# Performance work log

Hardware: AMD Instinct MI355X
Metric: run time of the kernel (lower is better)

Reference implementation:

```python
import jax, jax.numpy as jnp
import numpy as np

K_CHEB = 3  # Chebyshev order K -> K+1 basis matrices, gcn order = K


def setup_inputs() -> dict:
    key = jax.random.key(0)
    ks = jax.random.split(key, 7)
    B, N, T, Cin, Cout, ndim = 32, 512, 12, 64, 64, 40
    support_len = K_CHEB + 1
    cin_total = (K_CHEB * support_len + 1) * Cin  # (order*support_len+1)*c_in = 832
    x = jax.random.normal(ks[0], (B, N, T, Cin), jnp.float32)
    adj = (jax.random.uniform(ks[1], (N, N)) < 0.05).astype(jnp.float32)
    adjacency = jnp.maximum(adj, jnp.eye(N, dtype=jnp.float32))
    embedding = jax.random.uniform(ks[2], (N, ndim), dtype=jnp.float32)  # nn.init.uniform_
    W1 = jax.random.normal(ks[3], (ndim, ndim // 2), jnp.float32) * 0.3
    W2 = jax.random.normal(ks[4], (ndim, ndim // 2), jnp.float32) * 0.3
    mlp_w = jax.random.normal(ks[5], (Cout, cin_total), jnp.float32) / np.float32(np.sqrt(cin_total))
    mlp_b = jnp.zeros((Cout,), jnp.float32)
    return {"x": x, "adjacency": adjacency, "embedding": embedding,
            "W1": W1, "W2": W2, "mlp_w": mlp_w, "mlp_b": mlp_b}


def _cheb_kernels(adjacency, embedding, W1, W2):
    # adaptive adjacency: embedding mixed through column-softmaxed projections
    e1 = embedding @ jax.nn.softmax(W1, axis=0)
    e2 = embedding @ jax.nn.softmax(W2, axis=0)
    e1 = e1 / (jnp.linalg.norm(e1, axis=1, keepdims=True) + 1e-8)
    e2 = e2 / (jnp.linalg.norm(e2, axis=1, keepdims=True) + 1e-8)
    weight = e1 @ e2.T  # (N, N)
    A = jnp.where(adjacency > 0.0, weight + adjacency, jnp.asarray(9e-15, adjacency.dtype))
    # symmetric normalization: L = I - D^-1/2 A D^-1/2 ; Ls = (2/maxeig)*L - I with maxeig=2 -> Ls = -sym(A)
    d = 1.0 / jnp.sqrt(A.sum(axis=1))
    Ls = -(d[:, None] * A * d[None, :])
    I = jnp.eye(A.shape[0], dtype=A.dtype)
    kernels = [I, Ls]
    for _ in range(1, K_CHEB):  # Chebyshev recursion: T_{k+1} = 2 Ls T_k - T_{k-1}
        kernels.append(2.0 * (Ls @ kernels[-1]) - kernels[-2])
    return kernels  # K_CHEB + 1 matrices of (N, N)


def reference(x, adjacency, embedding, W1, W2, mlp_w, mlp_b):
    supports = _cheb_kernels(adjacency, embedding, W1, W2)
    xp = jnp.transpose(x, (0, 3, 1, 2))  # (B, Cin, N, T)
    out = [xp]
    for a in supports:
        x1 = jnp.einsum('bcvt,vw->bcwt', xp, a)
        out.append(x1)
        for _ in range(2, K_CHEB + 1):  # gcn order = K_CHEB
            x1 = jnp.einsum('bcvt,vw->bcwt', x1, a)
            out.append(x1)
    h = jnp.concatenate(out, axis=1)  # (B, 832, N, T)
    h = jnp.einsum('bcvt,oc->bovt', h, mlp_w) + mlp_b[None, :, None, None]  # 1x1 conv
    h = jnp.transpose(h, (0, 2, 3, 1))  # (B, N, T, Cout)
    return jax.nn.relu(h + x)  # conv_r is None (Cin == Cout), dropout eval no-op
```

## Files before the change

kernel.cpp:

```cpp
#include <hip/hip_runtime.h>
#include <hip/hip_bf16.h>

typedef unsigned short ushortT;
typedef unsigned int uintT;
typedef __attribute__((ext_vector_type(8))) short bf16x8;
typedef __attribute__((ext_vector_type(4))) float f32x4;
typedef __attribute__((ext_vector_type(4))) unsigned short us4;
typedef __attribute__((ext_vector_type(8))) unsigned short us8;

__device__ __forceinline__ ushortT f2bf(float f) {
    union { float f; uintT u; } x; x.f = f;
    uintT r = x.u + 0x7fffu + ((x.u >> 16) & 1u);
    return (ushortT)(r >> 16);
}
__device__ __forceinline__ float bf2f(ushortT u) {
    union { uintT u; float f; } x; x.u = ((uintT)u) << 16; return x.f;
}

#define ZLD 260
#define KTOT 5120

__global__ __launch_bounds__(256) void k_embed(const float* __restrict__ emb,
                                               const float* __restrict__ W1,
                                               const float* __restrict__ W2,
                                               float* __restrict__ e1,
                                               float* __restrict__ e2) {
    __shared__ float sW[800];
    __shared__ float sWs[800];
    const float* W = (blockIdx.x == 0) ? W1 : W2;
    float* e = (blockIdx.x == 0) ? e1 : e2;
    int tid = threadIdx.x;
    for (int i = tid; i < 800; i += 256) sW[i] = W[i];
    __syncthreads();
    if (tid < 20) {
        float mx = -1e30f;
        for (int i = 0; i < 40; ++i) mx = fmaxf(mx, sW[i * 20 + tid]);
        float s = 0.f;
        for (int i = 0; i < 40; ++i) s += __expf(sW[i * 20 + tid] - mx);
        float inv = 1.f / s;
        for (int i = 0; i < 40; ++i) sWs[i * 20 + tid] = __expf(sW[i * 20 + tid] - mx) * inv;
    }
    __syncthreads();
    for (int row = tid; row < 512; row += 256) {
        float acc[20];
        #pragma unroll
        for (int j = 0; j < 20; ++j) acc[j] = 0.f;
        for (int i = 0; i < 40; ++i) {
            float ev = emb[row * 40 + i];
            #pragma unroll
            for (int j = 0; j < 20; ++j) acc[j] += ev * sWs[i * 20 + j];
        }
        float s = 0.f;
        #pragma unroll
        for (int j = 0; j < 20; ++j) s += acc[j] * acc[j];
        float scale = 1.f / (sqrtf(s) + 1e-8f);
        #pragma unroll
        for (int j = 0; j < 20; ++j) e[row * 20 + j] = acc[j] * scale;
    }
}

__global__ __launch_bounds__(256) void k_adj(const float* __restrict__ adj,
                                             const float* __restrict__ e1,
                                             const float* __restrict__ e2,
                                             float* __restrict__ A,
                                             float* __restrict__ d) {
    int v = blockIdx.x, tid = threadIdx.x;
    __shared__ float ev[20];
    if (tid < 20) ev[tid] = e1[v * 20 + tid];
    __syncthreads();
    float local = 0.f;
    for (int w = tid; w < 512; w += 256) {
        float dot = 0.f;
        #pragma unroll
        for (int j = 0; j < 20; ++j) dot += ev[j] * e2[w * 20 + j];
        float av = adj[v * 512 + w];
        float Av = (av > 0.f) ? (dot + av) : 9e-15f;
        A[v * 512 + w] = Av;
        local += Av;
    }
    __shared__ float red[256];
    red[tid] = local;
    __syncthreads();
    for (int s = 128; s > 0; s >>= 1) {
        if (tid < s) red[tid] += red[tid + s];
        __syncthreads();
    }
    if (tid == 0) d[v] = 1.f / sqrtf(red[0]);
}

__global__ __launch_bounds__(256) void k_m(const float* __restrict__ A,
                                           const float* __restrict__ d,
                                           ushortT* __restrict__ P,
                                           const float* __restrict__ mlp_w,
                                           ushortT* __restrict__ Wq) {
    int bx = blockIdx.x, tid = threadIdx.x;
    if (bx < 512) {
        int w = bx;
        float dw = d[w];
        for (int v = tid; v < 512; v += 256) {
            float val = -d[v] * dw * A[v * 512 + w];
            P[512 * 512 + w * 512 + v] = f2bf(val);
            P[w * 512 + v] = (v == w) ? (ushortT)0x3F80 : (ushortT)0;
        }
    } else {
        int idx = (bx - 512) * 256 + tid;
        if (idx >= 10 * 64 * 64) return;
        int q = idx >> 12, rem = idx & 4095, o = rem >> 6, c = rem & 63;
        float v;
        if (q == 0) {
            v = 0.f;
            #pragma unroll
            for (int k = 0; k < 4; ++k) v += mlp_w[o * 832 + k * 64 + c];
        } else {
            v = mlp_w[o * 832 + (q + 3) * 64 + c];
        }
        Wq[idx] = f2bf(v);
    }
}

__global__ __launch_bounds__(256) void k_gemm512(const ushortT* __restrict__ A,
                                                 const ushortT* __restrict__ B,
                                                 ushortT* __restrict__ out1,
                                                 ushortT* __restrict__ out2,
                                                 int mode,
                                                 const ushortT* __restrict__ aux,
                                                 const ushortT* __restrict__ A2,
                                                 const ushortT* __restrict__ B2,
                                                 ushortT* __restrict__ out3) {
    int bx = blockIdx.x;
    if (bx >= 64) { A = A2; B = B2; out1 = out3; out2 = nullptr; mode = 0; bx -= 64; }
    int wave = threadIdx.x >> 6, lane = threadIdx.x & 63;
    int lr = lane & 15, lg = lane >> 4;
    int mbase = (bx >> 3) * 64;
    int nbase = (bx & 7) * 64 + wave * 16;
    f32x4 acc[4] = {};
    for (int kk = 0; kk < 16; ++kk) {
        int k0 = kk * 32 + lg * 8;
        bf16x8 bfr;
        #pragma unroll
        for (int j = 0; j < 8; ++j) bfr[j] = (short)B[(k0 + j) * 512 + nbase + lr];
        #pragma unroll
        for (int wt = 0; wt < 4; ++wt) {
            bf16x8 af = *(const bf16x8*)(A + (mbase + wt * 16 + lr) * 512 + k0);
            acc[wt] = __builtin_amdgcn_mfma_f32_16x16x32_bf16(af, bfr, acc[wt], 0, 0, 0);
        }
    }
    #pragma unroll
    for (int wt = 0; wt < 4; ++wt)
        #pragma unroll
        for (int r = 0; r < 4; ++r) {
            int row = mbase + wt * 16 + lg * 4 + r;
            int col = nbase + lr;
            float v = acc[wt][r];
            out1[row * 512 + col] = f2bf(v);
            if (mode == 1) out2[row * 512 + col] = f2bf(2.f * v - (row == col ? 1.f : 0.f));
            else if (mode == 2) out2[row * 512 + col] = f2bf(4.f * v - 3.f * bf2f(aux[row * 512 + col]));
        }
}

__global__ __launch_bounds__(256) void k_z(const float* __restrict__ x,
                                           const ushortT* __restrict__ Wq,
                                           ushortT* __restrict__ Z,
                                           int slab0) {
    __shared__ ushortT Zl[64 * ZLD];
    int bid = blockIdx.x;
    int btl = bid >> 1, chunk = bid & 1;
    int bt = slab0 + btl;
    int b = bt / 12, t = bt - b * 12;
    int tid = threadIdx.x, wave = tid >> 6, lane = tid & 63;
    int lr = lane & 15, lg = lane >> 4;

    bf16x8 xn[4][2];
    const float* xb = x + ((size_t)b * 512 * 12 + t) * 64;
    #pragma unroll
    for (int vt = 0; vt < 4; ++vt) {
        int vrow = chunk * 256 + wave * 64 + vt * 16 + lr;
        const float* px = xb + (size_t)vrow * 768 + lg * 8;
        f32x4 f0 = *(const f32x4*)px;
        f32x4 f1 = *(const f32x4*)(px + 4);
        f32x4 f2 = *(const f32x4*)(px + 32);
        f32x4 f3 = *(const f32x4*)(px + 36);
        bf16x8 v0, v1;
        v0[0] = (short)f2bf(f0[0]); v0[1] = (short)f2bf(f0[1]);
        v0[2] = (short)f2bf(f0[2]); v0[3] = (short)f2bf(f0[3]);
        v0[4] = (short)f2bf(f1[0]); v0[5] = (short)f2bf(f1[1]);
        v0[6] = (short)f2bf(f1[2]); v0[7] = (short)f2bf(f1[3]);
        v1[0] = (short)f2bf(f2[0]); v1[1] = (short)f2bf(f2[1]);
        v1[2] = (short)f2bf(f2[2]); v1[3] = (short)f2bf(f2[3]);
        v1[4] = (short)f2bf(f3[0]); v1[5] = (short)f2bf(f3[1]);
        v1[6] = (short)f2bf(f3[2]); v1[7] = (short)f2bf(f3[3]);
        xn[vt][0] = v0;
        xn[vt][1] = v1;
    }

    #pragma unroll 1
    for (int q = 0; q < 10; ++q) {
        const ushortT* wqp = Wq + q * 4096;
        #pragma unroll
        for (int ot = 0; ot < 4; ++ot) {
            int o = ot * 16 + lr;
            bf16x8 wf0 = *(const bf16x8*)(wqp + o * 64 + lg * 8);
            bf16x8 wf1 = *(const bf16x8*)(wqp + o * 64 + 32 + lg * 8);
            #pragma unroll
            for (int vt = 0; vt < 4; ++vt) {
                f32x4 z = {};
                z = __builtin_amdgcn_mfma_f32_16x16x32_bf16(xn[vt][0], wf0, z, 0, 0, 0);
                z = __builtin_amdgcn_mfma_f32_16x16x32_bf16(xn[vt][1], wf1, z, 0, 0, 0);
                us4 pk = { f2bf(z[0]), f2bf(z[1]), f2bf(z[2]), f2bf(z[3]) };
                *(us4*)&Zl[o * ZLD + wave * 64 + vt * 16 + lg * 4] = pk;
            }
        }
        __syncthreads();
        size_t kbase = (size_t)q * 512 + chunk * 256;
        #pragma unroll
        for (int j = 0; j < 8; ++j) {
            int flat = j * 256 + tid;
            int o = flat >> 5, slot = flat & 31;
            us4 lo = *(const us4*)&Zl[o * ZLD + slot * 8];
            us4 hi = *(const us4*)&Zl[o * ZLD + slot * 8 + 4];
            us8 val = { lo[0], lo[1], lo[2], lo[3], hi[0], hi[1], hi[2], hi[3] };
            *(us8*)&Z[(size_t)(btl * 64 + o) * KTOT + kbase + slot * 8] = val;
        }
        __syncthreads();
    }
}

__global__ __launch_bounds__(256) void k_big(const ushortT* __restrict__ P,
                                             const ushortT* __restrict__ Z,
                                             const float* __restrict__ x,
                                             const float* __restrict__ bias,
                                             float* __restrict__ out,
                                             int slab0) {
    __shared__ ushortT SA[3][4096];
    __shared__ ushortT SB[3][4096];
    int nwg = (int)gridDim.x;
    int bid = (int)blockIdx.x;
    int cpx = nwg >> 3;
    int lbid = (bid & 7) * cpx + (bid >> 3);
    int mblk = lbid & 3;
    int nblk = lbid >> 2;
    int mbase = mblk * 128;
    int n0 = nblk * 128;
    int tid = threadIdx.x, wave = tid >> 6, lane = tid & 63;
    int lr = lane & 15, lg = lane >> 4;
    int wm = wave >> 1, wn = wave & 1;
    int srow = tid >> 2, sg = tid & 3;

    f32x4 acc[4][4] = {};

    auto stage = [&](int kt, int buf) {
        int q = kt >> 4;
        int v0 = (kt & 15) * 32;
        const ushortT* Pk = P + (size_t)q * 262144 + v0 + sg * 8;
        const ushortT* Zk = Z + (size_t)kt * 32 + sg * 8;
        #pragma unroll
        for (int i = 0; i < 2; ++i) {
            int row = i * 64 + srow;
            __builtin_amdgcn_global_load_lds(Pk + (size_t)(mbase + row) * 512,
                                             &SA[buf][(i * 256 + wave * 64) * 8], 16, 0, 0);
            __builtin_amdgcn_global_load_lds(Zk + (size_t)(n0 + row) * KTOT,
                                             &SB[buf][(i * 256 + wave * 64) * 8], 16, 0, 0);
        }
    };

    auto phase = [&](int kt) {
        int buf = kt % 3;
        bf16x8 af[4], bfr[4];
        #pragma unroll
        for (int mt = 0; mt < 4; ++mt) {
            int m = wm * 64 + mt * 16 + lr;
            af[mt] = *(const bf16x8*)&SA[buf][m * 32 + lg * 8];
        }
        #pragma unroll
        for (int nt = 0; nt < 4; ++nt) {
            int n = wn * 64 + nt * 16 + lr;
            bfr[nt] = *(const bf16x8*)&SB[buf][n * 32 + lg * 8];
        }
        bool more = (kt + 2 < 160);
        if (more) stage(kt + 2, (kt + 2) % 3);
        asm volatile("s_waitcnt lgkmcnt(0)" ::: "memory");
        __builtin_amdgcn_sched_barrier(0);
        __builtin_amdgcn_s_setprio(1);
        #pragma unroll
        for (int mt = 0; mt < 4; ++mt)
            #pragma unroll
            for (int nt = 0; nt < 4; ++nt)
                acc[mt][nt] = __builtin_amdgcn_mfma_f32_16x16x32_bf16(af[mt], bfr[nt], acc[mt][nt], 0, 0, 0);
        __builtin_amdgcn_s_setprio(0);
        __builtin_amdgcn_sched_barrier(0);
        if (more) asm volatile("s_waitcnt vmcnt(4)" ::: "memory");
        else      asm volatile("s_waitcnt vmcnt(0)" ::: "memory");
        __builtin_amdgcn_sched_barrier(0);
        __builtin_amdgcn_s_barrier();
        __builtin_amdgcn_sched_barrier(0);
    };

    stage(0, 0);
    stage(1, 1);
    asm volatile("s_waitcnt vmcnt(0)" ::: "memory");
    __builtin_amdgcn_sched_barrier(0);
    __builtin_amdgcn_s_barrier();
    __builtin_amdgcn_sched_barrier(0);

    #pragma unroll 1
    for (int kt = 0; kt < 160; ++kt) phase(kt);

    #pragma unroll
    for (int mt = 0; mt < 4; ++mt)
        #pragma unroll
        for (int nt = 0; nt < 4; ++nt)
            #pragma unroll
            for (int r = 0; r < 4; ++r) {
                int m = mbase + wm * 64 + mt * 16 + lg * 4 + r;
                int nf = n0 + wn * 64 + nt * 16 + lr;
                int btl = nf >> 6, o = nf & 63;
                int bt = slab0 + btl;
                int bb = bt / 12, t = bt - bb * 12;
                size_t oi = (((size_t)bb * 512 + m) * 12 + t) * 64 + o;
                float v = acc[mt][nt][r] + x[oi] + bias[o];
                out[oi] = (v > 0.f) ? v : 0.f;
            }
}

__global__ __launch_bounds__(256, 2) void k_main_fb(const float* __restrict__ x,
                                                    const ushortT* __restrict__ P,
                                                    const ushortT* __restrict__ Wq,
                                                    const float* __restrict__ bias,
                                                    float* __restrict__ out) {
    __shared__ ushortT Zt[64 * ZLD];
    const int SZ = 512 * 512;
    int bid = blockIdx.x;
    int slot = bid & 7, idx = bid >> 3;
    int half = slot >> 2;
    int bt = idx * 4 + (slot & 3);
    int b = bt / 12, tt = bt - b * 12;
    int tid = threadIdx.x, wave = tid >> 6, lane = tid & 63;
    int lr = lane & 15, lg = lane >> 4;
    int wbase = half * 256 + wave * 64;
    int vzb = wave * 64;
    const float* xqf = x + ((size_t)b * 512 * 12 + tt) * 64;

    f32x4 oacc[4][4] = {};
    bf16x8 xn[4][2];

    auto xload = [&](int ch) {
        #pragma unroll
        for (int vt = 0; vt < 4; ++vt) {
            int vrow = ch * 256 + vzb + vt * 16 + lr;
            const float* px = xqf + (size_t)vrow * 768 + lg * 8;
            f32x4 f0 = *(const f32x4*)px;
            f32x4 f1 = *(const f32x4*)(px + 4);
            f32x4 f2 = *(const f32x4*)(px + 32);
            f32x4 f3 = *(const f32x4*)(px + 36);
            bf16x8 v0, v1;
            v0[0] = (short)f2bf(f0[0]); v0[1] = (short)f2bf(f0[1]);
            v0[2] = (short)f2bf(f0[2]); v0[3] = (short)f2bf(f0[3]);
            v0[4] = (short)f2bf(f1[0]); v0[5] = (short)f2bf(f1[1]);
            v0[6] = (short)f2bf(f1[2]); v0[7] = (short)f2bf(f1[3]);
            v1[0] = (short)f2bf(f2[0]); v1[1] = (short)f2bf(f2[1]);
            v1[2] = (short)f2bf(f2[2]); v1[3] = (short)f2bf(f2[3]);
            v1[4] = (short)f2bf(f3[0]); v1[5] = (short)f2bf(f3[1]);
            v1[6] = (short)f2bf(f3[2]); v1[7] = (short)f2bf(f3[3]);
            xn[vt][0] = v0;
            xn[vt][1] = v1;
        }
    };
    auto zphase = [&](int q) {
        const ushortT* wqp = Wq + q * 4096;
        #pragma unroll
        for (int vt = 0; vt < 4; ++vt)
            #pragma unroll
            for (int ot = 0; ot < 4; ++ot) {
                int o = ot * 16 + lr;
                bf16x8 wf0 = *(const bf16x8*)(wqp + o * 64 + lg * 8);
                bf16x8 wf1 = *(const bf16x8*)(wqp + o * 64 + 32 + lg * 8);
                f32x4 z = {};
                z = __builtin_amdgcn_mfma_f32_16x16x32_bf16(xn[vt][0], wf0, z, 0, 0, 0);
                z = __builtin_amdgcn_mfma_f32_16x16x32_bf16(xn[vt][1], wf1, z, 0, 0, 0);
                us4 pk = { f2bf(z[0]), f2bf(z[1]), f2bf(z[2]), f2bf(z[3]) };
                *(us4*)&Zt[o * ZLD + vzb + vt * 16 + lg * 4] = pk;
            }
    };
    auto pptr = [&](int j, int mt) -> const ushortT* {
        int q = 1 + (j >> 1), ch = j & 1;
        return P + (size_t)q * SZ + (size_t)(wbase + mt * 16 + lr) * 512 + ch * 256 + lg * 8;
    };

    xload(half);
    zphase(0);
    xload(0);
    __syncthreads();
    #pragma unroll
    for (int mt = 0; mt < 4; ++mt)
        #pragma unroll
        for (int ot = 0; ot < 4; ++ot) {
            int o = ot * 16 + lr;
            us4 z4 = *(const us4*)&Zt[o * ZLD + wave * 64 + mt * 16 + lg * 4];
            oacc[mt][ot][0] = bf2f(z4[0]);
            oacc[mt][ot][1] = bf2f(z4[1]);
            oacc[mt][ot][2] = bf2f(z4[2]);
            oacc[mt][ot][3] = bf2f(z4[3]);
        }
    __syncthreads();

    #pragma unroll 1
    for (int j = 0; j < 18; ++j) {
        int q = 1 + (j >> 1);
        zphase(q);
        int jn = (j < 17) ? j + 1 : 17;
        xload(jn & 1);
        __syncthreads();
        const ushortT* pc0 = pptr(j, 0);
        const ushortT* pc1 = pptr(j, 1);
        const ushortT* pc2 = pptr(j, 2);
        const ushortT* pc3 = pptr(j, 3);
        #pragma unroll
        for (int kk = 0; kk < 8; ++kk) {
            bf16x8 a0 = *(const bf16x8*)(pc0 + kk * 32);
            bf16x8 a1 = *(const bf16x8*)(pc1 + kk * 32);
            bf16x8 a2 = *(const bf16x8*)(pc2 + kk * 32);
            bf16x8 a3 = *(const bf16x8*)(pc3 + kk * 32);
            int vb = kk * 32 + lg * 8;
            bf16x8 b0 = *(const bf16x8*)&Zt[(0 * 16 + lr) * ZLD + vb];
            bf16x8 b1 = *(const bf16x8*)&Zt[(1 * 16 + lr) * ZLD + vb];
            bf16x8 b2 = *(const bf16x8*)&Zt[(2 * 16 + lr) * ZLD + vb];
            bf16x8 b3 = *(const bf16x8*)&Zt[(3 * 16 + lr) * ZLD + vb];
            oacc[0][0] = __builtin_amdgcn_mfma_f32_16x16x32_bf16(a0, b0, oacc[0][0], 0, 0, 0);
            oacc[1][0] = __builtin_amdgcn_mfma_f32_16x16x32_bf16(a1, b0, oacc[1][0], 0, 0, 0);
            oacc[2][0] = __builtin_amdgcn_mfma_f32_16x16x32_bf16(a2, b0, oacc[2][0], 0, 0, 0);
            oacc[3][0] = __builtin_amdgcn_mfma_f32_16x16x32_bf16(a3, b0, oacc[3][0], 0, 0, 0);
            oacc[0][1] = __builtin_amdgcn_mfma_f32_16x16x32_bf16(a0, b1, oacc[0][1], 0, 0, 0);
            oacc[1][1] = __builtin_amdgcn_mfma_f32_16x16x32_bf16(a1, b1, oacc[1][1], 0, 0, 0);
            oacc[2][1] = __builtin_amdgcn_mfma_f32_16x16x32_bf16(a2, b1, oacc[2][1], 0, 0, 0);
            oacc[3][1] = __builtin_amdgcn_mfma_f32_16x16x32_bf16(a3, b1, oacc[3][1], 0, 0, 0);
            oacc[0][2] = __builtin_amdgcn_mfma_f32_16x16x32_bf16(a0, b2, oacc[0][2], 0, 0, 0);
            oacc[1][2] = __builtin_amdgcn_mfma_f32_16x16x32_bf16(a1, b2, oacc[1][2], 0, 0, 0);
            oacc[2][2] = __builtin_amdgcn_mfma_f32_16x16x32_bf16(a2, b2, oacc[2][2], 0, 0, 0);
            oacc[3][2] = __builtin_amdgcn_mfma_f32_16x16x32_bf16(a3, b2, oacc[3][2], 0, 0, 0);
            oacc[0][3] = __builtin_amdgcn_mfma_f32_16x16x32_bf16(a0, b3, oacc[0][3], 0, 0, 0);
            oacc[1][3] = __builtin_amdgcn_mfma_f32_16x16x32_bf16(a1, b3, oacc[1][3], 0, 0, 0);
            oacc[2][3] = __builtin_amdgcn_mfma_f32_16x16x32_bf16(a2, b3, oacc[2][3], 0, 0, 0);
            oacc[3][3] = __builtin_amdgcn_mfma_f32_16x16x32_bf16(a3, b3, oacc[3][3], 0, 0, 0);
        }
        __syncthreads();
    }

    #pragma unroll
    for (int mt = 0; mt < 4; ++mt)
        #pragma unroll
        for (int ot = 0; ot < 4; ++ot)
            #pragma unroll
            for (int r = 0; r < 4; ++r) {
                int w = wbase + mt * 16 + lg * 4 + r;
                int o = ot * 16 + lr;
                size_t oi = (((size_t)b * 512 + w) * 12 + tt) * 64 + o;
                float v = oacc[mt][ot][r] + x[oi] + bias[o];
                out[oi] = (v > 0.f) ? v : 0.f;
            }
}

extern "C" void kernel_launch(void* const* d_in, const int* in_sizes, int n_in,
                              void* d_out, int out_size, void* d_ws, size_t ws_size,
                              hipStream_t stream) {
    const float* x    = (const float*)d_in[0];
    const float* adj  = (const float*)d_in[1];
    const float* emb  = (const float*)d_in[2];
    const float* W1   = (const float*)d_in[3];
    const float* W2   = (const float*)d_in[4];
    const float* mlpw = (const float*)d_in[5];
    const float* mlpb = (const float*)d_in[6];
    float* out = (float*)d_out;

    char* ws = (char*)d_ws;
    float*   e1   = (float*)(ws + 0);
    float*   e2   = (float*)(ws + 65536);
    float*   A    = (float*)(ws + 131072);
    float*   dvec = (float*)(ws + 1179648);
    ushortT* P    = (ushortT*)(ws + 1183744);
    ushortT* Wq   = (ushortT*)(ws + 6426624);
    ushortT* Z    = (ushortT*)(ws + 6508544);
    const size_t ZOFF = 6508544;

    k_embed<<<2, 256, 0, stream>>>(emb, W1, W2, e1, e2);
    k_adj<<<512, 256, 0, stream>>>(adj, e1, e2, A, dvec);
    k_m<<<672, 256, 0, stream>>>(A, dvec, P, mlpw, Wq);

    const int SZ = 512 * 512;
    ushortT *S1 = P + 1 * SZ, *S2 = P + 2 * SZ, *S3 = P + 3 * SZ, *S4 = P + 4 * SZ,
            *S5 = P + 5 * SZ, *S6 = P + 6 * SZ, *S7 = P + 7 * SZ, *S8 = P + 8 * SZ,
            *S9 = P + 9 * SZ;
    k_gemm512<<<64, 256, 0, stream>>>(S1, S1, S2, S4, 1, nullptr, nullptr, nullptr, nullptr);
    k_gemm512<<<128, 256, 0, stream>>>(S1, S2, S3, S7, 2, S1, S4, S4, S5);
    k_gemm512<<<128, 256, 0, stream>>>(S4, S5, S6, nullptr, 0, nullptr, S7, S7, S8);
    k_gemm512<<<64, 256, 0, stream>>>(S7, S8, S9, nullptr, 0, nullptr, nullptr, nullptr, nullptr);

    const size_t ZFULL = (size_t)24576 * KTOT * 2;
    int nslab = 1;
    while (nslab <= 8 && ws_size < ZOFF + ZFULL / (size_t)nslab) nslab <<= 1;

    if (nslab <= 8) {
        int btps = 384 / nslab;
        for (int s = 0; s < nslab; ++s) {
            k_z<<<btps * 2, 256, 0, stream>>>(x, Wq, Z, s * btps);
            k_big<<<btps * 2, 256, 0, stream>>>(P, Z, x, mlpb, out, s * btps);
        }
    } else {
        k_main_fb<<<768, 256, 0, stream>>>(x, P, Wq, mlpb, out);
    }
    (void)in_sizes; (void)n_in; (void)out_size;
}
```

Baseline: 373.0 us.

## Deepen k_big pipeline to four LDS buffers and pre-convert x to bf16

The main GEMM kernel moves from a 3-stage to a 4-stage LDS ring, prefetching three k-tiles ahead and placing the vmcnt wait and barrier at the start of each phase, so global loads get more time to land before use. A new prep kernel converts x to bf16 in a (bt, v, c) layout when the workspace is large enough, so k_z reads contiguous bf16 rows instead of strided fp32 with inline conversion. The costs are more LDS per block (64KB), which may lower occupancy, an extra kernel launch, and a full extra pass over x.

```diff
diff --git a/kernel.cpp b/kernel.cpp
--- a/kernel.cpp
+++ b/kernel.cpp
@@ -118,6 +118,101 @@
     }
 }
 
+__global__ __launch_bounds__(256) void k_prep(const float* __restrict__ x,
+                                              ushortT* __restrict__ xbf) {
+    size_t i = (size_t)blockIdx.x * 256 + threadIdx.x;
+    int c = (int)(i & 15) * 4;
+    int v = (int)((i >> 4) & 511);
+    int bt = (int)(i >> 13);
+    int b = bt / 12, t = bt - b * 12;
+    f32x4 f = *(const f32x4*)(x + (((size_t)b * 512 + v) * 12 + t) * 64 + c);
+    us4 o = { f2bf(f[0]), f2bf(f[1]), f2bf(f[2]), f2bf(f[3]) };
+    *(us4*)(xbf + ((size_t)bt * 512 + v) * 64 + c) = o;
+}
+
+template<bool XBF>
+__device__ void kz_body(const float* __restrict__ x,
+                        const ushortT* __restrict__ xbf,
+                        const ushortT* __restrict__ Wq,
+                        ushortT* __restrict__ Z,
+                        int kzbid, int slab0) {
+    __shared__ ushortT Zl[64 * ZLD];
+    int btl = kzbid >> 1, chunk = kzbid & 1;
+    int bt = slab0 + btl;
+    int b = bt / 12, t = bt - b * 12;
+    int tid = threadIdx.x, wave = tid >> 6, lane = tid & 63;
+    int lr = lane & 15, lg = lane >> 4;
+
+    bf16x8 xn[4][2];
+    const float* xb = x + ((size_t)b * 512 * 12 + t) * 64;
+    const ushortT* xq = xbf + (size_t)bt * 512 * 64;
+    #pragma unroll
+    for (int vt = 0; vt < 4; ++vt) {
+        int vrow = chunk * 256 + wave * 64 + vt * 16 + lr;
+        if (XBF) {
+            xn[vt][0] = *(const bf16x8*)(xq + vrow * 64 + lg * 8);
+            xn[vt][1] = *(const bf16x8*)(xq + vrow * 64 + 32 + lg * 8);
+        } else {
+            const float* px = xb + (size_t)vrow * 768 + lg * 8;
+            f32x4 f0 = *(const f32x4*)px;
+            f32x4 f1 = *(const f32x4*)(px + 4);
+            f32x4 f2 = *(const f32x4*)(px + 32);
+            f32x4 f3 = *(const f32x4*)(px + 36);
+            bf16x8 v0, v1;
+            v0[0] = (short)f2bf(f0[0]); v0[1] = (short)f2bf(f0[1]);
+            v0[2] = (short)f2bf(f0[2]); v0[3] = (short)f2bf(f0[3]);
+            v0[4] = (short)f2bf(f1[0]); v0[5] = (short)f2bf(f1[1]);
+            v0[6] = (short)f2bf(f1[2]); v0[7] = (short)f2bf(f1[3]);
+            v1[0] = (short)f2bf(f2[0]); v1[1] = (short)f2bf(f2[1]);
+            v1[2] = (short)f2bf(f2[2]); v1[3] = (short)f2bf(f2[3]);
+            v1[4] = (short)f2bf(f3[0]); v1[5] = (short)f2bf(f3[1]);
+            v1[6] = (short)f2bf(f3[2]); v1[7] = (short)f2bf(f3[3]);
+            xn[vt][0] = v0;
+            xn[vt][1] = v1;
+        }
+    }
+
+    #pragma unroll 1
+    for (int q = 0; q < 10; ++q) {
+        const ushortT* wqp = Wq + q * 4096;
+        #pragma unroll
+        for (int ot = 0; ot < 4; ++ot) {
+            int o = ot * 16 + lr;
+            bf16x8 wf0 = *(const bf16x8*)(wqp + o * 64 + lg * 8);
+            bf16x8 wf1 = *(const bf16x8*)(wqp + o * 64 + 32 + lg * 8);
+            #pragma unroll
+            for (int vt = 0; vt < 4; ++vt) {
+                f32x4 z = {};
+                z = __builtin_amdgcn_mfma_f32_16x16x32_bf16(xn[vt][0], wf0, z, 0, 0, 0);
+                z = __builtin_amdgcn_mfma_f32_16x16x32_bf16(xn[vt][1], wf1, z, 0, 0, 0);
+                us4 pk = { f2bf(z[0]), f2bf(z[1]), f2bf(z[2]), f2bf(z[3]) };
+                *(us4*)&Zl[o * ZLD + wave * 64 + vt * 16 + lg * 4] = pk;
+            }
+        }
+        __syncthreads();
+        size_t kbase = (size_t)q * 512 + chunk * 256;
+        #pragma unroll
+        for (int j = 0; j < 8; ++j) {
+            int flat = j * 256 + tid;
+            int o = flat >> 5, slot = flat & 31;
+            us4 lo = *(const us4*)&Zl[o * ZLD + slot * 8];
+            us4 hi = *(const us4*)&Zl[o * ZLD + slot * 8 + 4];
+            us8 val = { lo[0], lo[1], lo[2], lo[3], hi[0], hi[1], hi[2], hi[3] };
+            *(us8*)&Z[(size_t)(btl * 64 + o) * KTOT + kbase + slot * 8] = val;
+        }
+        __syncthreads();
+    }
+}
+
+template<bool XBF>
+__global__ __launch_bounds__(256) void k_z(const float* __restrict__ x,
+                                           const ushortT* __restrict__ xbf,
+                                           const ushortT* __restrict__ Wq,
+                                           ushortT* __restrict__ Z,
+                                           int slab0) {
+    kz_body<XBF>(x, xbf, Wq, Z, blockIdx.x, slab0);
+}
+
 __global__ __launch_bounds__(256) void k_gemm512(const ushortT* __restrict__ A,
                                                  const ushortT* __restrict__ B,
                                                  ushortT* __restrict__ out1,
@@ -158,81 +253,14 @@
         }
 }
 
-__global__ __launch_bounds__(256) void k_z(const float* __restrict__ x,
-                                           const ushortT* __restrict__ Wq,
-                                           ushortT* __restrict__ Z,
-                                           int slab0) {
-    __shared__ ushortT Zl[64 * ZLD];
-    int bid = blockIdx.x;
-    int btl = bid >> 1, chunk = bid & 1;
-    int bt = slab0 + btl;
-    int b = bt / 12, t = bt - b * 12;
-    int tid = threadIdx.x, wave = tid >> 6, lane = tid & 63;
-    int lr = lane & 15, lg = lane >> 4;
-
-    bf16x8 xn[4][2];
-    const float* xb = x + ((size_t)b * 512 * 12 + t) * 64;
-    #pragma unroll
-    for (int vt = 0; vt < 4; ++vt) {
-        int vrow = chunk * 256 + wave * 64 + vt * 16 + lr;
-        const float* px = xb + (size_t)vrow * 768 + lg * 8;
-        f32x4 f0 = *(const f32x4*)px;
-        f32x4 f1 = *(const f32x4*)(px + 4);
-        f32x4 f2 = *(const f32x4*)(px + 32);
-        f32x4 f3 = *(const f32x4*)(px + 36);
-        bf16x8 v0, v1;
-        v0[0] = (short)f2bf(f0[0]); v0[1] = (short)f2bf(f0[1]);
-        v0[2] = (short)f2bf(f0[2]); v0[3] = (short)f2bf(f0[3]);
-        v0[4] = (short)f2bf(f1[0]); v0[5] = (short)f2bf(f1[1]);
-        v0[6] = (short)f2bf(f1[2]); v0[7] = (short)f2bf(f1[3]);
-        v1[0] = (short)f2bf(f2[0]); v1[1] = (short)f2bf(f2[1]);
-        v1[2] = (short)f2bf(f2[2]); v1[3] = (short)f2bf(f2[3]);
-        v1[4] = (short)f2bf(f3[0]); v1[5] = (short)f2bf(f3[1]);
-        v1[6] = (short)f2bf(f3[2]); v1[7] = (short)f2bf(f3[3]);
-        xn[vt][0] = v0;
-        xn[vt][1] = v1;
-    }
-
-    #pragma unroll 1
-    for (int q = 0; q < 10; ++q) {
-        const ushortT* wqp = Wq + q * 4096;
-        #pragma unroll
-        for (int ot = 0; ot < 4; ++ot) {
-            int o = ot * 16 + lr;
-            bf16x8 wf0 = *(const bf16x8*)(wqp + o * 64 + lg * 8);
-            bf16x8 wf1 = *(const bf16x8*)(wqp + o * 64 + 32 + lg * 8);
-            #pragma unroll
-            for (int vt = 0; vt < 4; ++vt) {
-                f32x4 z = {};
-                z = __builtin_amdgcn_mfma_f32_16x16x32_bf16(xn[vt][0], wf0, z, 0, 0, 0);
-                z = __builtin_amdgcn_mfma_f32_16x16x32_bf16(xn[vt][1], wf1, z, 0, 0, 0);
-                us4 pk = { f2bf(z[0]), f2bf(z[1]), f2bf(z[2]), f2bf(z[3]) };
-                *(us4*)&Zl[o * ZLD + wave * 64 + vt * 16 + lg * 4] = pk;
-            }
-        }
-        __syncthreads();
-        size_t kbase = (size_t)q * 512 + chunk * 256;
-        #pragma unroll
-        for (int j = 0; j < 8; ++j) {
-            int flat = j * 256 + tid;
-            int o = flat >> 5, slot = flat & 31;
-            us4 lo = *(const us4*)&Zl[o * ZLD + slot * 8];
-            us4 hi = *(const us4*)&Zl[o * ZLD + slot * 8 + 4];
-            us8 val = { lo[0], lo[1], lo[2], lo[3], hi[0], hi[1], hi[2], hi[3] };
-            *(us8*)&Z[(size_t)(btl * 64 + o) * KTOT + kbase + slot * 8] = val;
-        }
-        __syncthreads();
-    }
-}
-
 __global__ __launch_bounds__(256) void k_big(const ushortT* __restrict__ P,
                                              const ushortT* __restrict__ Z,
                                              const float* __restrict__ x,
                                              const float* __restrict__ bias,
                                              float* __restrict__ out,
                                              int slab0) {
-    __shared__ ushortT SA[3][4096];
-    __shared__ ushortT SB[3][4096];
+    __shared__ ushortT SA[4][4096];
+    __shared__ ushortT SB[4][4096];
     int nwg = (int)gridDim.x;
     int bid = (int)blockIdx.x;
     int cpx = nwg >> 3;
@@ -263,8 +291,14 @@
         }
     };
 
-    auto phase = [&](int kt) {
-        int buf = kt % 3;
+    auto phase = [&](int kt, int wsel) {
+        if (wsel == 0)      asm volatile("s_waitcnt vmcnt(8)" ::: "memory");
+        else if (wsel == 1) asm volatile("s_waitcnt vmcnt(4)" ::: "memory");
+        else                asm volatile("s_waitcnt vmcnt(0)" ::: "memory");
+        __builtin_amdgcn_sched_barrier(0);
+        __builtin_amdgcn_s_barrier();
+        __builtin_amdgcn_sched_barrier(0);
+        int buf = kt & 3;
         bf16x8 af[4], bfr[4];
         #pragma unroll
         for (int mt = 0; mt < 4; ++mt) {
@@ -276,10 +310,7 @@
             int n = wn * 64 + nt * 16 + lr;
             bfr[nt] = *(const bf16x8*)&SB[buf][n * 32 + lg * 8];
         }
-        bool more = (kt + 2 < 160);
-        if (more) stage(kt + 2, (kt + 2) % 3);
-        asm volatile("s_waitcnt lgkmcnt(0)" ::: "memory");
-        __builtin_amdgcn_sched_barrier(0);
+        if (kt + 3 < 160) stage(kt + 3, (kt + 3) & 3);
         __builtin_amdgcn_s_setprio(1);
         #pragma unroll
         for (int mt = 0; mt < 4; ++mt)
@@ -288,22 +319,19 @@
                 acc[mt][nt] = __builtin_amdgcn_mfma_f32_16x16x32_bf16(af[mt], bfr[nt], acc[mt][nt], 0, 0, 0);
         __builtin_amdgcn_s_setprio(0);
         __builtin_amdgcn_sched_barrier(0);
-        if (more) asm volatile("s_waitcnt vmcnt(4)" ::: "memory");
-        else      asm volatile("s_waitcnt vmcnt(0)" ::: "memory");
-        __builtin_amdgcn_sched_barrier(0);
-        __builtin_amdgcn_s_barrier();
-        __builtin_amdgcn_sched_barrier(0);
     };
 
     stage(0, 0);
+    __builtin_amdgcn_sched_barrier(0);
     stage(1, 1);
-    asm volatile("s_waitcnt vmcnt(0)" ::: "memory");
     __builtin_amdgcn_sched_barrier(0);
-    __builtin_amdgcn_s_barrier();
+    stage(2, 2);
     __builtin_amdgcn_sched_barrier(0);
 
     #pragma unroll 1
-    for (int kt = 0; kt < 160; ++kt) phase(kt);
+    for (int kt = 0; kt < 158; ++kt) phase(kt, 0);
+    phase(158, 1);
+    phase(159, 2);
 
     #pragma unroll
     for (int mt = 0; mt < 4; ++mt)
@@ -480,7 +508,15 @@
     ushortT* Wq   = (ushortT*)(ws + 6426624);
     ushortT* Z    = (ushortT*)(ws + 6508544);
     const size_t ZOFF = 6508544;
-
+    const size_t ZFULL = (size_t)24576 * KTOT * 2;
+    const size_t XBFSZ = (size_t)384 * 512 * 64 * 2;
+    ushortT* xbf = (ushortT*)(ws + ZOFF + ZFULL);
+
+    int nslab = 1;
+    while (nslab <= 8 && ws_size < ZOFF + ZFULL / (size_t)nslab) nslab <<= 1;
+    const bool use_xbf = (nslab == 1) && (ws_size >= ZOFF + ZFULL + XBFSZ);
+
+    if (use_xbf) k_prep<<<12288, 256, 0, stream>>>(x, xbf);
     k_embed<<<2, 256, 0, stream>>>(emb, W1, W2, e1, e2);
     k_adj<<<512, 256, 0, stream>>>(adj, e1, e2, A, dvec);
     k_m<<<672, 256, 0, stream>>>(A, dvec, P, mlpw, Wq);
@@ -494,14 +530,13 @@
     k_gemm512<<<128, 256, 0, stream>>>(S4, S5, S6, nullptr, 0, nullptr, S7, S7, S8);
     k_gemm512<<<64, 256, 0, stream>>>(S7, S8, S9, nullptr, 0, nullptr, nullptr, nullptr, nullptr);
 
-    const size_t ZFULL = (size_t)24576 * KTOT * 2;
-    int nslab = 1;
-    while (nslab <= 8 && ws_size < ZOFF + ZFULL / (size_t)nslab) nslab <<= 1;
-
     if (nslab <= 8) {
         int btps = 384 / nslab;
         for (int s = 0; s < nslab; ++s) {
-            k_z<<<btps * 2, 256, 0, stream>>>(x, Wq, Z, s * btps);
+            if (use_xbf)
+                k_z<true><<<btps * 2, 256, 0, stream>>>(x, xbf, Wq, Z, s * btps);
+            else
+                k_z<false><<<btps * 2, 256, 0, stream>>>(x, nullptr, Wq, Z, s * btps);
             k_big<<<btps * 2, 256, 0, stream>>>(P, Z, x, mlpb, out, s * btps);
         }
     } else {
```

Result: no change. 375.1 us (+0.6%).
